# Optimization experiments

Hardware: AMD Instinct MI355X
Metric: run time of the kernel (lower is better)

Reference implementation:

```python
import jax, jax.numpy as jnp
import numpy as np

LN_EPS = 1e-5  # torch LayerNorm default


def layer_norm(x, g, b):
    m = jnp.mean(x, axis=-1, keepdims=True)
    v = jnp.mean((x - m) ** 2, axis=-1, keepdims=True)
    return (x - m) / jnp.sqrt(v + LN_EPS) * g + b


def scatter_mean(src, idx, n):
    # src: [E, h], idx: [E] -> [n, h], mean with count clamped to >= 1
    s = jax.ops.segment_sum(src, idx, num_segments=n)
    cnt = jax.ops.segment_sum(jnp.ones((src.shape[0],), src.dtype), idx, num_segments=n)
    return s / jnp.clip(cnt, 1.0)[:, None]


def setup_inputs() -> dict:
    key = jax.random.key(0)
    ks = jax.random.split(key, 16)
    N, C, E, h = 200000, 50000, 600000, 128

    def w(k, shape, fan_in):
        return (jax.random.normal(k, shape, jnp.float32) / np.float32(np.sqrt(fan_in)))

    ci = jax.random.randint(ks[2], (E,), 0, C)
    vi = jax.random.randint(ks[3], (E,), 0, N)
    return {
        "vh": jax.random.normal(ks[0], (N, h), jnp.float32),
        "ch": jax.random.normal(ks[1], (C, h), jnp.float32),
        "edge_index": jnp.stack([ci, vi]).astype(jnp.int64),
        "ew": jax.random.normal(ks[4], (E,), jnp.float32),
        "v2c_lin_w": w(ks[5], (h, h), h), "v2c_lin_b": jnp.zeros((h,), jnp.float32),
        "v2c_gate_w": w(ks[6], (h, 1), 1), "v2c_gate_b": jnp.zeros((h,), jnp.float32),
        "v2c_upd_w": w(ks[7], (h, 2 * h), 2 * h), "v2c_upd_b": jnp.zeros((h,), jnp.float32),
        "v2c_ln_g": jnp.ones((h,), jnp.float32), "v2c_ln_b": jnp.zeros((h,), jnp.float32),
        "c2v_lin_w": w(ks[8], (h, h), h), "c2v_lin_b": jnp.zeros((h,), jnp.float32),
        "c2v_gate_w": w(ks[9], (h, 1), 1), "c2v_gate_b": jnp.zeros((h,), jnp.float32),
        "c2v_upd_w": w(ks[10], (h, 2 * h), 2 * h), "c2v_upd_b": jnp.zeros((h,), jnp.float32),
        "c2v_ln_g": jnp.ones((h,), jnp.float32), "c2v_ln_b": jnp.zeros((h,), jnp.float32),
    }


def reference(vh, ch, edge_index, ew,
              v2c_lin_w, v2c_lin_b, v2c_gate_w, v2c_gate_b,
              v2c_upd_w, v2c_upd_b, v2c_ln_g, v2c_ln_b,
              c2v_lin_w, c2v_lin_b, c2v_gate_w, c2v_gate_b,
              c2v_upd_w, c2v_upd_b, c2v_ln_g, c2v_ln_b):
    ci, vi = edge_index[0], edge_index[1]
    e = ew[:, None]  # [E, 1]

    # var -> con
    gate = jax.nn.sigmoid(e @ v2c_gate_w.T + v2c_gate_b)          # [E, h]
    msg = (vh @ v2c_lin_w.T + v2c_lin_b)[vi] * gate               # gather + gate
    agg = scatter_mean(msg, ci, ch.shape[0])                      # [C, h]
    ch_new = jax.nn.relu(layer_norm(
        jnp.concatenate([agg, ch], -1) @ v2c_upd_w.T + v2c_upd_b,
        v2c_ln_g, v2c_ln_b))

    # con -> var (uses updated ch)
    gate = jax.nn.sigmoid(e @ c2v_gate_w.T + c2v_gate_b)
    msg = (ch_new @ c2v_lin_w.T + c2v_lin_b)[ci] * gate
    agg = scatter_mean(msg, vi, vh.shape[0])                      # [N, h]
    vh_new = jax.nn.relu(layer_norm(
        jnp.concatenate([agg, vh], -1) @ c2v_upd_w.T + c2v_upd_b,
        c2v_ln_g, c2v_ln_b))

    return vh_new, ch_new
```

## Files before the change

kernel.cpp:

```cpp
#include <hip/hip_runtime.h>

#define LN_EPS 1e-5f

typedef float f32x4 __attribute__((ext_vector_type(4)));
typedef short bf16x8 __attribute__((ext_vector_type(8)));
typedef unsigned short u16x4 __attribute__((ext_vector_type(4)));

__device__ __forceinline__ unsigned short f2bf(float f) {
  unsigned int u = __float_as_uint(f);
  u = (u + 0x7fffu + ((u >> 16) & 1u)) >> 16;
  return (unsigned short)u;
}
__device__ __forceinline__ float bf2f(unsigned short h) {
  return __uint_as_float((unsigned int)h << 16);
}
__device__ __forceinline__ float sigm(float x) {
  return 1.f / (1.f + __expf(-x));
}

__global__ __launch_bounds__(256) void cvt4_bf16(const float* __restrict__ a,
                                                 const float* __restrict__ b,
                                                 const float* __restrict__ c,
                                                 const float* __restrict__ d,
                                                 unsigned short* __restrict__ oa,
                                                 unsigned short* __restrict__ ob,
                                                 unsigned short* __restrict__ oc,
                                                 unsigned short* __restrict__ od) {
  int i = blockIdx.x * 256 + threadIdx.x;
  if (i < 16384) oa[i] = f2bf(a[i]);
  else if (i < 49152) ob[i - 16384] = f2bf(b[i - 16384]);
  else if (i < 65536) oc[i - 49152] = f2bf(c[i - 49152]);
  else if (i < 98304) od[i - 65536] = f2bf(d[i - 65536]);
}

__global__ __launch_bounds__(256) void hist2_rank(const int* __restrict__ ci,
                                                  const int* __restrict__ vi,
                                                  int* __restrict__ cntC,
                                                  int* __restrict__ cntV,
                                                  int* __restrict__ rankC,
                                                  int* __restrict__ rankV, int E) {
  int tid = blockIdx.x * 256 + threadIdx.x;
  int T = gridDim.x * 256;
  int e[4], c[4], v[4];
  bool ok[4];
#pragma unroll
  for (int i = 0; i < 4; ++i) {
    e[i] = tid + i * T;
    ok[i] = e[i] < E;
  }
#pragma unroll
  for (int i = 0; i < 4; ++i) if (ok[i]) c[i] = ci[e[i]];
#pragma unroll
  for (int i = 0; i < 4; ++i) if (ok[i]) v[i] = vi[e[i]];
  int rc[4], rv[4];
#pragma unroll
  for (int i = 0; i < 4; ++i) if (ok[i]) rc[i] = atomicAdd(&cntC[c[i]], 1);
#pragma unroll
  for (int i = 0; i < 4; ++i) if (ok[i]) rv[i] = atomicAdd(&cntV[v[i]], 1);
#pragma unroll
  for (int i = 0; i < 4; ++i) if (ok[i]) rankC[e[i]] = rc[i];
#pragma unroll
  for (int i = 0; i < 4; ++i) if (ok[i]) rankV[e[i]] = rv[i];
}

__global__ __launch_bounds__(256) void scan1(const int* __restrict__ cnt,
                                             int* __restrict__ off,
                                             int* __restrict__ bsum, int M) {
  __shared__ int s[256];
  int base = blockIdx.x * 1024 + threadIdx.x * 4;
  int v[4];
  int tot = 0;
#pragma unroll
  for (int i = 0; i < 4; ++i) {
    int idx = base + i;
    v[i] = (idx < M) ? cnt[idx] : 0;
    tot += v[i];
  }
  s[threadIdx.x] = tot;
  __syncthreads();
  for (int d = 1; d < 256; d <<= 1) {
    int t = (threadIdx.x >= d) ? s[threadIdx.x - d] : 0;
    __syncthreads();
    s[threadIdx.x] += t;
    __syncthreads();
  }
  int excl = s[threadIdx.x] - tot;
#pragma unroll
  for (int i = 0; i < 4; ++i) {
    int idx = base + i;
    if (idx < M) off[idx] = excl;
    excl += v[i];
  }
  if (threadIdx.x == 255) bsum[blockIdx.x] = s[255];
}

__global__ __launch_bounds__(256) void scan2(int* __restrict__ bsum, int nb) {
  __shared__ int s[256];
  __shared__ int carry;
  if (threadIdx.x == 0) carry = 0;
  __syncthreads();
  for (int base = 0; base < nb; base += 256) {
    int idx = base + threadIdx.x;
    int v = (idx < nb) ? bsum[idx] : 0;
    s[threadIdx.x] = v;
    __syncthreads();
    for (int d = 1; d < 256; d <<= 1) {
      int t = (threadIdx.x >= d) ? s[threadIdx.x - d] : 0;
      __syncthreads();
      s[threadIdx.x] += t;
      __syncthreads();
    }
    if (idx < nb) bsum[idx] = s[threadIdx.x] - v + carry;
    __syncthreads();
    if (threadIdx.x == 0) carry += s[255];
    __syncthreads();
  }
}

__global__ __launch_bounds__(256) void scan3(int* __restrict__ off,
                                             const int* __restrict__ bsum, int M, int E) {
  int idx = blockIdx.x * 256 + threadIdx.x;
  if (idx < M) off[idx] += bsum[idx >> 10];
  if (idx == M) off[M] = E;
}

__global__ __launch_bounds__(256) void scatter2_kernel(const int* __restrict__ ci,
                                                       const int* __restrict__ vi,
                                                       const float* __restrict__ ew,
                                                       const int* __restrict__ offC,
                                                       const int* __restrict__ offV,
                                                       const int* __restrict__ rankC,
                                                       const int* __restrict__ rankV,
                                                       int2* __restrict__ edataC,
                                                       int2* __restrict__ edataV, int E) {
  int tid = blockIdx.x * 256 + threadIdx.x;
  int T = gridDim.x * 256;
  int e[4], c[4], v[4], wb[4], rc[4], rv[4];
  bool ok[4];
#pragma unroll
  for (int i = 0; i < 4; ++i) {
    e[i] = tid + i * T;
    ok[i] = e[i] < E;
  }
#pragma unroll
  for (int i = 0; i < 4; ++i) if (ok[i]) c[i] = ci[e[i]];
#pragma unroll
  for (int i = 0; i < 4; ++i) if (ok[i]) v[i] = vi[e[i]];
#pragma unroll
  for (int i = 0; i < 4; ++i) if (ok[i]) wb[i] = __float_as_int(ew[e[i]]);
#pragma unroll
  for (int i = 0; i < 4; ++i) if (ok[i]) rc[i] = rankC[e[i]];
#pragma unroll
  for (int i = 0; i < 4; ++i) if (ok[i]) rv[i] = rankV[e[i]];
  int pc[4], pv[4];
#pragma unroll
  for (int i = 0; i < 4; ++i) if (ok[i]) pc[i] = offC[c[i]] + rc[i];
#pragma unroll
  for (int i = 0; i < 4; ++i) if (ok[i]) pv[i] = offV[v[i]] + rv[i];
#pragma unroll
  for (int i = 0; i < 4; ++i) if (ok[i]) edataC[pc[i]] = make_int2(v[i], wb[i]);
#pragma unroll
  for (int i = 0; i < 4; ++i) if (ok[i]) edataV[pv[i]] = make_int2(c[i], wb[i]);
}

__global__ __launch_bounds__(256) void seg_reduce(const int* __restrict__ off,
                                                  const int2* __restrict__ edata,
                                                  const float* __restrict__ gw,
                                                  const float* __restrict__ gb,
                                                  const unsigned short* __restrict__ src,
                                                  int srcStride,
                                                  unsigned short* __restrict__ out,
                                                  int outStride, int M) {
  int seg = blockIdx.x * 4 + (threadIdx.x >> 6);
  if (seg >= M) return;
  int j = threadIdx.x & 63;
  int start = off[seg], end = off[seg + 1];
  float gwa = gw[2 * j], gwb = gw[2 * j + 1];
  float gba = gb[2 * j], gbb = gb[2 * j + 1];
  float a0 = 0.f, a1 = 0.f;
  int p = start;
  for (; p + 4 <= end; p += 4) {
    int2 e0 = edata[p], e1 = edata[p + 1], e2 = edata[p + 2], e3 = edata[p + 3];
    unsigned int v0 = *reinterpret_cast<const unsigned int*>(&src[(size_t)e0.x * srcStride + 2 * j]);
    unsigned int v1 = *reinterpret_cast<const unsigned int*>(&src[(size_t)e1.x * srcStride + 2 * j]);
    unsigned int v2 = *reinterpret_cast<const unsigned int*>(&src[(size_t)e2.x * srcStride + 2 * j]);
    unsigned int v3 = *reinterpret_cast<const unsigned int*>(&src[(size_t)e3.x * srcStride + 2 * j]);
    float w0 = __int_as_float(e0.y), w1 = __int_as_float(e1.y);
    float w2 = __int_as_float(e2.y), w3 = __int_as_float(e3.y);
    a0 += bf2f((unsigned short)(v0 & 0xffff)) * sigm(w0 * gwa + gba)
        + bf2f((unsigned short)(v1 & 0xffff)) * sigm(w1 * gwa + gba)
        + bf2f((unsigned short)(v2 & 0xffff)) * sigm(w2 * gwa + gba)
        + bf2f((unsigned short)(v3 & 0xffff)) * sigm(w3 * gwa + gba);
    a1 += bf2f((unsigned short)(v0 >> 16)) * sigm(w0 * gwb + gbb)
        + bf2f((unsigned short)(v1 >> 16)) * sigm(w1 * gwb + gbb)
        + bf2f((unsigned short)(v2 >> 16)) * sigm(w2 * gwb + gbb)
        + bf2f((unsigned short)(v3 >> 16)) * sigm(w3 * gwb + gbb);
  }
  if (p + 2 <= end) {
    int2 e0 = edata[p], e1 = edata[p + 1];
    unsigned int v0 = *reinterpret_cast<const unsigned int*>(&src[(size_t)e0.x * srcStride + 2 * j]);
    unsigned int v1 = *reinterpret_cast<const unsigned int*>(&src[(size_t)e1.x * srcStride + 2 * j]);
    float w0 = __int_as_float(e0.y), w1 = __int_as_float(e1.y);
    a0 += bf2f((unsigned short)(v0 & 0xffff)) * sigm(w0 * gwa + gba)
        + bf2f((unsigned short)(v1 & 0xffff)) * sigm(w1 * gwa + gba);
    a1 += bf2f((unsigned short)(v0 >> 16)) * sigm(w0 * gwb + gbb)
        + bf2f((unsigned short)(v1 >> 16)) * sigm(w1 * gwb + gbb);
    p += 2;
  }
  if (p < end) {
    int2 e0 = edata[p];
    unsigned int v0 = *reinterpret_cast<const unsigned int*>(&src[(size_t)e0.x * srcStride + 2 * j]);
    float w0 = __int_as_float(e0.y);
    a0 += bf2f((unsigned short)(v0 & 0xffff)) * sigm(w0 * gwa + gba);
    a1 += bf2f((unsigned short)(v0 >> 16)) * sigm(w0 * gwb + gbb);
  }
  int cnt = end - start;
  float inv = 1.f / (float)(cnt > 1 ? cnt : 1);
  unsigned int packed = (unsigned int)f2bf(a0 * inv) | ((unsigned int)f2bf(a1 * inv) << 16);
  *reinterpret_cast<unsigned int*>(&out[(size_t)seg * outStride + 2 * j]) = packed;
}

template <int K, int OS, bool WBF>
__global__ __launch_bounds__(256) void gemm_lin_mfma(const float* __restrict__ X,
                                                     const unsigned short* __restrict__ Wbf,
                                                     const float* __restrict__ bias,
                                                     unsigned short* __restrict__ out,
                                                     unsigned short* __restrict__ bfdst,
                                                     int M) {
  __shared__ unsigned short Xs[64][40];
  __shared__ unsigned short Bs[128][40];
  const int tid = threadIdx.x;
  const int lane = tid & 63, wv = tid >> 6;
  const int lr = lane & 15, lg = lane >> 4;
  const int row0 = blockIdx.x * 64;

  f32x4 acc[4][2];
#pragma unroll
  for (int mf = 0; mf < 4; ++mf)
#pragma unroll
    for (int nf = 0; nf < 2; ++nf) acc[mf][nf] = (f32x4)(0.f);

  for (int k0 = 0; k0 < K; k0 += 32) {
#pragma unroll
    for (int it = 0; it < 2; ++it) {
      int q = tid + it * 256;
      int r = q >> 3, kq = (q & 7) * 4;
      int grow = row0 + r;
      float4 v = make_float4(0.f, 0.f, 0.f, 0.f);
      if (grow < M) v = *reinterpret_cast<const float4*>(&X[(size_t)grow * K + k0 + kq]);
      u16x4 p = {f2bf(v.x), f2bf(v.y), f2bf(v.z), f2bf(v.w)};
      *reinterpret_cast<u16x4*>(&Xs[r][kq]) = p;
      if (WBF && grow < M)
        *reinterpret_cast<u16x4*>(&bfdst[(size_t)grow * 256 + 128 + k0 + kq]) = p;
    }
#pragma unroll
    for (int it = 0; it < 2; ++it) {
      int q = tid + it * 256;
      int n = q >> 2, kq = (q & 3) * 8;
      bf16x8 wrow = *reinterpret_cast<const bf16x8*>(&Wbf[(size_t)n * K + k0 + kq]);
      *reinterpret_cast<bf16x8*>(&Bs[n][kq]) = wrow;
    }
    __syncthreads();
    bf16x8 a[4], b[2];
#pragma unroll
    for (int mf = 0; mf < 4; ++mf)
      a[mf] = *reinterpret_cast<const bf16x8*>(&Xs[mf * 16 + lr][lg * 8]);
#pragma unroll
    for (int nf = 0; nf < 2; ++nf)
      b[nf] = *reinterpret_cast<const bf16x8*>(&Bs[wv * 32 + nf * 16 + lr][lg * 8]);
#pragma unroll
    for (int mf = 0; mf < 4; ++mf)
#pragma unroll
      for (int nf = 0; nf < 2; ++nf)
        acc[mf][nf] = __builtin_amdgcn_mfma_f32_16x16x32_bf16(a[mf], b[nf], acc[mf][nf], 0, 0, 0);
    __syncthreads();
  }

  int col[2];
  float bv[2];
#pragma unroll
  for (int nf = 0; nf < 2; ++nf) {
    col[nf] = wv * 32 + nf * 16 + lr;
    bv[nf] = bias[col[nf]];
  }
#pragma unroll
  for (int mf = 0; mf < 4; ++mf)
#pragma unroll
    for (int reg = 0; reg < 4; ++reg) {
      int grow = row0 + mf * 16 + lg * 4 + reg;
      if (grow < M) {
#pragma unroll
        for (int nf = 0; nf < 2; ++nf)
          out[(size_t)grow * OS + col[nf]] = f2bf(acc[mf][nf][reg] + bv[nf]);
      }
    }
}

__global__ __launch_bounds__(256) void gemm_upd_mix(const unsigned short* __restrict__ agg,
                                                    const float* __restrict__ base,
                                                    const unsigned short* __restrict__ Wbf,
                                                    const float* __restrict__ bias,
                                                    const float* __restrict__ lng,
                                                    const float* __restrict__ lnb,
                                                    float* __restrict__ out, int M) {
  constexpr int K = 256;
  __shared__ unsigned short Xs[64][40];
  __shared__ unsigned short Bs[128][40];
  __shared__ float sredS[64][4];
  __shared__ float sredQ[64][4];
  const int tid = threadIdx.x;
  const int lane = tid & 63, wv = tid >> 6;
  const int lr = lane & 15, lg = lane >> 4;
  const int row0 = blockIdx.x * 64;

  f32x4 acc[4][2];
#pragma unroll
  for (int mf = 0; mf < 4; ++mf)
#pragma unroll
    for (int nf = 0; nf < 2; ++nf) acc[mf][nf] = (f32x4)(0.f);

  for (int k0 = 0; k0 < K; k0 += 32) {
#pragma unroll
    for (int it = 0; it < 2; ++it) {
      int q = tid + it * 256;
      int r = q >> 3, kq = (q & 7) * 4;
      int grow = row0 + r, gk = k0 + kq;
      u16x4 p = {0, 0, 0, 0};
      if (grow < M) {
        if (gk < 128) {
          p = *reinterpret_cast<const u16x4*>(&agg[(size_t)grow * 128 + gk]);
        } else {
          float4 v = *reinterpret_cast<const float4*>(&base[(size_t)grow * 128 + (gk - 128)]);
          p = {f2bf(v.x), f2bf(v.y), f2bf(v.z), f2bf(v.w)};
        }
      }
      *reinterpret_cast<u16x4*>(&Xs[r][kq]) = p;
    }
#pragma unroll
    for (int it = 0; it < 2; ++it) {
      int q = tid + it * 256;
      int n = q >> 2, kq = (q & 3) * 8;
      bf16x8 wrow = *reinterpret_cast<const bf16x8*>(&Wbf[(size_t)n * K + k0 + kq]);
      *reinterpret_cast<bf16x8*>(&Bs[n][kq]) = wrow;
    }
    __syncthreads();
    bf16x8 a[4], b[2];
#pragma unroll
    for (int mf = 0; mf < 4; ++mf)
      a[mf] = *reinterpret_cast<const bf16x8*>(&Xs[mf * 16 + lr][lg * 8]);
#pragma unroll
    for (int nf = 0; nf < 2; ++nf)
      b[nf] = *reinterpret_cast<const bf16x8*>(&Bs[wv * 32 + nf * 16 + lr][lg * 8]);
#pragma unroll
    for (int mf = 0; mf < 4; ++mf)
#pragma unroll
      for (int nf = 0; nf < 2; ++nf)
        acc[mf][nf] = __builtin_amdgcn_mfma_f32_16x16x32_bf16(a[mf], b[nf], acc[mf][nf], 0, 0, 0);
    __syncthreads();
  }

  int col[2];
  float bv[2], gv[2], lv[2];
#pragma unroll
  for (int nf = 0; nf < 2; ++nf) {
    col[nf] = wv * 32 + nf * 16 + lr;
    bv[nf] = bias[col[nf]];
    gv[nf] = lng[col[nf]];
    lv[nf] = lnb[col[nf]];
  }

  float z[4][4][2];
#pragma unroll
  for (int mf = 0; mf < 4; ++mf)
#pragma unroll
    for (int reg = 0; reg < 4; ++reg) {
      float z0 = acc[mf][0][reg] + bv[0];
      float z1 = acc[mf][1][reg] + bv[1];
      z[mf][reg][0] = z0;
      z[mf][reg][1] = z1;
      float s = z0 + z1;
      float q = z0 * z0 + z1 * z1;
#pragma unroll
      for (int m = 1; m < 16; m <<= 1) {
        s += __shfl_xor(s, m);
        q += __shfl_xor(q, m);
      }
      if (lr == 0) {
        sredS[mf * 16 + lg * 4 + reg][wv] = s;
        sredQ[mf * 16 + lg * 4 + reg][wv] = q;
      }
    }
  __syncthreads();
#pragma unroll
  for (int mf = 0; mf < 4; ++mf)
#pragma unroll
    for (int reg = 0; reg < 4; ++reg) {
      int tr = mf * 16 + lg * 4 + reg;
      f32x4 S4 = *reinterpret_cast<const f32x4*>(&sredS[tr][0]);
      f32x4 Q4 = *reinterpret_cast<const f32x4*>(&sredQ[tr][0]);
      float S = S4[0] + S4[1] + S4[2] + S4[3];
      float Q = Q4[0] + Q4[1] + Q4[2] + Q4[3];
      float mean = S * (1.f / 128.f);
      float var = Q * (1.f / 128.f) - mean * mean;
      float rstd = rsqrtf(var + LN_EPS);
      int grow = row0 + tr;
      if (grow < M) {
#pragma unroll
        for (int nf = 0; nf < 2; ++nf) {
          float y = (z[mf][reg][nf] - mean) * rstd * gv[nf] + lv[nf];
          out[(size_t)grow * 128 + col[nf]] = fmaxf(y, 0.f);
        }
      }
    }
}

__global__ __launch_bounds__(256) void gemm_upd_cat(const unsigned short* __restrict__ Xc,
                                                    const unsigned short* __restrict__ Wbf,
                                                    const float* __restrict__ bias,
                                                    const float* __restrict__ lng,
                                                    const float* __restrict__ lnb,
                                                    float* __restrict__ out, int M) {
  constexpr int K = 256;
  __shared__ unsigned short Xs[64][40];
  __shared__ unsigned short Bs[128][40];
  __shared__ float sredS[64][4];
  __shared__ float sredQ[64][4];
  const int tid = threadIdx.x;
  const int lane = tid & 63, wv = tid >> 6;
  const int lr = lane & 15, lg = lane >> 4;
  const int row0 = blockIdx.x * 64;

  f32x4 acc[4][2];
#pragma unroll
  for (int mf = 0; mf < 4; ++mf)
#pragma unroll
    for (int nf = 0; nf < 2; ++nf) acc[mf][nf] = (f32x4)(0.f);

  for (int k0 = 0; k0 < K; k0 += 32) {
#pragma unroll
    for (int it = 0; it < 2; ++it) {
      int q = tid + it * 256;
      int r = q >> 3, kq = (q & 7) * 4;
      int grow = row0 + r;
      u16x4 p = {0, 0, 0, 0};
      if (grow < M) p = *reinterpret_cast<const u16x4*>(&Xc[(size_t)grow * 256 + k0 + kq]);
      *reinterpret_cast<u16x4*>(&Xs[r][kq]) = p;
    }
#pragma unroll
    for (int it = 0; it < 2; ++it) {
      int q = tid + it * 256;
      int n = q >> 2, kq = (q & 3) * 8;
      bf16x8 wrow = *reinterpret_cast<const bf16x8*>(&Wbf[(size_t)n * K + k0 + kq]);
      *reinterpret_cast<bf16x8*>(&Bs[n][kq]) = wrow;
    }
    __syncthreads();
    bf16x8 a[4], b[2];
#pragma unroll
    for (int mf = 0; mf < 4; ++mf)
      a[mf] = *reinterpret_cast<const bf16x8*>(&Xs[mf * 16 + lr][lg * 8]);
#pragma unroll
    for (int nf = 0; nf < 2; ++nf)
      b[nf] = *reinterpret_cast<const bf16x8*>(&Bs[wv * 32 + nf * 16 + lr][lg * 8]);
#pragma unroll
    for (int mf = 0; mf < 4; ++mf)
#pragma unroll
      for (int nf = 0; nf < 2; ++nf)
        acc[mf][nf] = __builtin_amdgcn_mfma_f32_16x16x32_bf16(a[mf], b[nf], acc[mf][nf], 0, 0, 0);
    __syncthreads();
  }

  int col[2];
  float bv[2], gv[2], lv[2];
#pragma unroll
  for (int nf = 0; nf < 2; ++nf) {
    col[nf] = wv * 32 + nf * 16 + lr;
    bv[nf] = bias[col[nf]];
    gv[nf] = lng[col[nf]];
    lv[nf] = lnb[col[nf]];
  }

  float z[4][4][2];
#pragma unroll
  for (int mf = 0; mf < 4; ++mf)
#pragma unroll
    for (int reg = 0; reg < 4; ++reg) {
      float z0 = acc[mf][0][reg] + bv[0];
      float z1 = acc[mf][1][reg] + bv[1];
      z[mf][reg][0] = z0;
      z[mf][reg][1] = z1;
      float s = z0 + z1;
      float q = z0 * z0 + z1 * z1;
#pragma unroll
      for (int m = 1; m < 16; m <<= 1) {
        s += __shfl_xor(s, m);
        q += __shfl_xor(q, m);
      }
      if (lr == 0) {
        sredS[mf * 16 + lg * 4 + reg][wv] = s;
        sredQ[mf * 16 + lg * 4 + reg][wv] = q;
      }
    }
  __syncthreads();
#pragma unroll
  for (int mf = 0; mf < 4; ++mf)
#pragma unroll
    for (int reg = 0; reg < 4; ++reg) {
      int tr = mf * 16 + lg * 4 + reg;
      f32x4 S4 = *reinterpret_cast<const f32x4*>(&sredS[tr][0]);
      f32x4 Q4 = *reinterpret_cast<const f32x4*>(&sredQ[tr][0]);
      float S = S4[0] + S4[1] + S4[2] + S4[3];
      float Q = Q4[0] + Q4[1] + Q4[2] + Q4[3];
      float mean = S * (1.f / 128.f);
      float var = Q * (1.f / 128.f) - mean * mean;
      float rstd = rsqrtf(var + LN_EPS);
      int grow = row0 + tr;
      if (grow < M) {
#pragma unroll
        for (int nf = 0; nf < 2; ++nf) {
          float y = (z[mf][reg][nf] - mean) * rstd * gv[nf] + lv[nf];
          out[(size_t)grow * 128 + col[nf]] = fmaxf(y, 0.f);
        }
      }
    }
}

extern "C" void kernel_launch(void* const* d_in, const int* in_sizes, int n_in,
                              void* d_out, int out_size, void* d_ws, size_t ws_size,
                              hipStream_t stream) {
  const float* vh = (const float*)d_in[0];
  const float* ch = (const float*)d_in[1];
  const int* ei = (const int*)d_in[2];
  const float* ew = (const float*)d_in[3];
  const float* v2c_lin_w = (const float*)d_in[4];
  const float* v2c_lin_b = (const float*)d_in[5];
  const float* v2c_gate_w = (const float*)d_in[6];
  const float* v2c_gate_b = (const float*)d_in[7];
  const float* v2c_upd_w = (const float*)d_in[8];
  const float* v2c_upd_b = (const float*)d_in[9];
  const float* v2c_ln_g = (const float*)d_in[10];
  const float* v2c_ln_b = (const float*)d_in[11];
  const float* c2v_lin_w = (const float*)d_in[12];
  const float* c2v_lin_b = (const float*)d_in[13];
  const float* c2v_gate_w = (const float*)d_in[14];
  const float* c2v_gate_b = (const float*)d_in[15];
  const float* c2v_upd_w = (const float*)d_in[16];
  const float* c2v_upd_b = (const float*)d_in[17];
  const float* c2v_ln_g = (const float*)d_in[18];
  const float* c2v_ln_b = (const float*)d_in[19];

  const int N = in_sizes[0] / 128;
  const int C = in_sizes[1] / 128;
  const int E = in_sizes[3];
  const int* ci = ei;
  const int* vi = ei + E;

  unsigned short* Xcat = (unsigned short*)d_ws;
  unsigned short* aggC = Xcat + (size_t)N * 256;
  unsigned short* wbf = aggC + (size_t)C * 128;
  unsigned short* wbfLinV = wbf;
  unsigned short* wbfUpdV = wbf + 16384;
  unsigned short* wbfLinC = wbf + 49152;
  unsigned short* wbfUpdC = wbf + 65536;
  int* offC = (int*)(wbf + 98304);
  int* offV = offC + (C + 1);
  size_t ofs = (size_t)((offV + (N + 1)) - (int*)d_ws);
  ofs = (ofs + 1) & ~(size_t)1;
  int2* edataC = (int2*)((int*)d_ws + ofs);
  int2* edataV = edataC + E;
  int* cntC = (int*)aggC;
  int* cntV = cntC + C;
  int* bsumS = cntV + N;
  int* rankC = bsumS + 1024;
  int* rankV = rankC + E;

  float* vhNew = (float*)d_out;
  float* chNew = (float*)d_out + (size_t)N * 128;

  cvt4_bf16<<<(98304 + 255) / 256, 256, 0, stream>>>(v2c_lin_w, v2c_upd_w, c2v_lin_w,
                                                     c2v_upd_w, wbfLinV, wbfUpdV, wbfLinC,
                                                     wbfUpdC);

  const int egrid4 = (E + 4 * 256 - 1) / (4 * 256);

  hipMemsetAsync(cntC, 0, (size_t)(C + N) * sizeof(int), stream);
  hist2_rank<<<egrid4, 256, 0, stream>>>(ci, vi, cntC, cntV, rankC, rankV, E);
  {
    int nb = (C + 1023) / 1024;
    scan1<<<nb, 256, 0, stream>>>(cntC, offC, bsumS, C);
    scan2<<<1, 256, 0, stream>>>(bsumS, nb);
    scan3<<<(C + 1 + 255) / 256, 256, 0, stream>>>(offC, bsumS, C, E);
  }
  {
    int nb = (N + 1023) / 1024;
    scan1<<<nb, 256, 0, stream>>>(cntV, offV, bsumS, N);
    scan2<<<1, 256, 0, stream>>>(bsumS, nb);
    scan3<<<(N + 1 + 255) / 256, 256, 0, stream>>>(offV, bsumS, N, E);
  }
  scatter2_kernel<<<egrid4, 256, 0, stream>>>(ci, vi, ew, offC, offV, rankC, rankV,
                                              edataC, edataV, E);

  gemm_lin_mfma<128, 256, true><<<(N + 63) / 64, 256, 0, stream>>>(vh, wbfLinV, v2c_lin_b,
                                                                   Xcat, Xcat, N);
  seg_reduce<<<(C + 3) / 4, 256, 0, stream>>>(offC, edataC, v2c_gate_w, v2c_gate_b,
                                              Xcat, 256, aggC, 128, C);
  gemm_upd_mix<<<(C + 63) / 64, 256, 0, stream>>>(aggC, ch, wbfUpdV, v2c_upd_b,
                                                  v2c_ln_g, v2c_ln_b, chNew, C);

  unsigned short* tmpC = aggC;
  gemm_lin_mfma<128, 128, false><<<(C + 63) / 64, 256, 0, stream>>>(chNew, wbfLinC,
                                                                    c2v_lin_b, tmpC,
                                                                    nullptr, C);
  seg_reduce<<<(N + 3) / 4, 256, 0, stream>>>(offV, edataV, c2v_gate_w, c2v_gate_b,
                                              tmpC, 128, Xcat, 256, N);
  gemm_upd_cat<<<(N + 63) / 64, 256, 0, stream>>>(Xcat, wbfUpdC, c2v_upd_b,
                                                  c2v_ln_g, c2v_ln_b, vhNew, N);
}
```

Measured before the change: 355.0 us.

## Restructure GEMMs to keep A fragments in registers and stage full weight in LDS

Replaces the K-looped shared-memory GEMMs with kernels where each wave loads its 16 rows of A directly into registers as MFMA fragments and the whole weight matrix (or half of it) is staged once into LDS. Each wave now covers all 128 output columns, so the LayerNorm row reduction is done with in-wave shuffles and no longer needs the cross-wave shared-memory reduction or the per-K-step barriers. The update GEMM uses 512-thread blocks of 128 rows. This trades larger LDS use (about 34KB per block) and more registers for fewer barriers and less A traffic through LDS, which may lower occupancy.

```diff
diff --git a/kernel.cpp b/kernel.cpp
--- a/kernel.cpp
+++ b/kernel.cpp
@@ -220,308 +220,192 @@
   *reinterpret_cast<unsigned int*>(&out[(size_t)seg * outStride + 2 * j]) = packed;
 }
 
-template <int K, int OS, bool WBF>
-__global__ __launch_bounds__(256) void gemm_lin_mfma(const float* __restrict__ X,
-                                                     const unsigned short* __restrict__ Wbf,
-                                                     const float* __restrict__ bias,
-                                                     unsigned short* __restrict__ out,
-                                                     unsigned short* __restrict__ bfdst,
-                                                     int M) {
-  __shared__ unsigned short Xs[64][40];
-  __shared__ unsigned short Bs[128][40];
+template <int OS, bool WBF>
+__global__ __launch_bounds__(256) void gemm_lin_reg(const float* __restrict__ X,
+                                                    const unsigned short* __restrict__ Wbf,
+                                                    const float* __restrict__ bias,
+                                                    unsigned short* __restrict__ out,
+                                                    unsigned short* __restrict__ bfdst,
+                                                    int M) {
+  __shared__ unsigned short Bs[128][136];
   const int tid = threadIdx.x;
   const int lane = tid & 63, wv = tid >> 6;
   const int lr = lane & 15, lg = lane >> 4;
-  const int row0 = blockIdx.x * 64;
-
-  f32x4 acc[4][2];
-#pragma unroll
-  for (int mf = 0; mf < 4; ++mf)
-#pragma unroll
-    for (int nf = 0; nf < 2; ++nf) acc[mf][nf] = (f32x4)(0.f);
-
-  for (int k0 = 0; k0 < K; k0 += 32) {
-#pragma unroll
-    for (int it = 0; it < 2; ++it) {
-      int q = tid + it * 256;
-      int r = q >> 3, kq = (q & 7) * 4;
-      int grow = row0 + r;
-      float4 v = make_float4(0.f, 0.f, 0.f, 0.f);
-      if (grow < M) v = *reinterpret_cast<const float4*>(&X[(size_t)grow * K + k0 + kq]);
-      u16x4 p = {f2bf(v.x), f2bf(v.y), f2bf(v.z), f2bf(v.w)};
-      *reinterpret_cast<u16x4*>(&Xs[r][kq]) = p;
-      if (WBF && grow < M)
-        *reinterpret_cast<u16x4*>(&bfdst[(size_t)grow * 256 + 128 + k0 + kq]) = p;
-    }
-#pragma unroll
-    for (int it = 0; it < 2; ++it) {
-      int q = tid + it * 256;
-      int n = q >> 2, kq = (q & 3) * 8;
-      bf16x8 wrow = *reinterpret_cast<const bf16x8*>(&Wbf[(size_t)n * K + k0 + kq]);
-      *reinterpret_cast<bf16x8*>(&Bs[n][kq]) = wrow;
-    }
-    __syncthreads();
-    bf16x8 a[4], b[2];
-#pragma unroll
-    for (int mf = 0; mf < 4; ++mf)
-      a[mf] = *reinterpret_cast<const bf16x8*>(&Xs[mf * 16 + lr][lg * 8]);
-#pragma unroll
-    for (int nf = 0; nf < 2; ++nf)
-      b[nf] = *reinterpret_cast<const bf16x8*>(&Bs[wv * 32 + nf * 16 + lr][lg * 8]);
-#pragma unroll
-    for (int mf = 0; mf < 4; ++mf)
-#pragma unroll
-      for (int nf = 0; nf < 2; ++nf)
-        acc[mf][nf] = __builtin_amdgcn_mfma_f32_16x16x32_bf16(a[mf], b[nf], acc[mf][nf], 0, 0, 0);
-    __syncthreads();
-  }
-
-  int col[2];
-  float bv[2];
-#pragma unroll
-  for (int nf = 0; nf < 2; ++nf) {
-    col[nf] = wv * 32 + nf * 16 + lr;
-    bv[nf] = bias[col[nf]];
-  }
-#pragma unroll
-  for (int mf = 0; mf < 4; ++mf)
+  const int row0 = blockIdx.x * 64 + wv * 16;
+
+  const int arow = row0 + lr;
+  const bool rowok = arow < M;
+  const float* xrow = X + (size_t)arow * 128;
+
+  float4 x0[4], x1[4];
+#pragma unroll
+  for (int ks = 0; ks < 4; ++ks) {
+    int kb = ks * 32 + lg * 8;
+    if (rowok) {
+      x0[ks] = *reinterpret_cast<const float4*>(xrow + kb);
+      x1[ks] = *reinterpret_cast<const float4*>(xrow + kb + 4);
+    } else {
+      x0[ks] = make_float4(0.f, 0.f, 0.f, 0.f);
+      x1[ks] = x0[ks];
+    }
+  }
+
+#pragma unroll
+  for (int it = 0; it < 8; ++it) {
+    int q = tid + it * 256;
+    int n = q >> 4, kq = (q & 15) * 8;
+    *reinterpret_cast<bf16x8*>(&Bs[n][kq]) =
+        *reinterpret_cast<const bf16x8*>(&Wbf[(size_t)n * 128 + kq]);
+  }
+
+  bf16x8 a[4];
+#pragma unroll
+  for (int ks = 0; ks < 4; ++ks) {
+    a[ks] = (bf16x8){(short)f2bf(x0[ks].x), (short)f2bf(x0[ks].y),
+                     (short)f2bf(x0[ks].z), (short)f2bf(x0[ks].w),
+                     (short)f2bf(x1[ks].x), (short)f2bf(x1[ks].y),
+                     (short)f2bf(x1[ks].z), (short)f2bf(x1[ks].w)};
+    if (WBF && rowok)
+      *reinterpret_cast<bf16x8*>(&bfdst[(size_t)arow * 256 + 128 + ks * 32 + lg * 8]) = a[ks];
+  }
+  __syncthreads();
+
+  f32x4 acc[8];
+#pragma unroll
+  for (int nf = 0; nf < 8; ++nf) acc[nf] = (f32x4)(0.f);
+#pragma unroll
+  for (int ks = 0; ks < 4; ++ks) {
+#pragma unroll
+    for (int nf = 0; nf < 8; ++nf) {
+      bf16x8 b = *reinterpret_cast<const bf16x8*>(&Bs[nf * 16 + lr][ks * 32 + lg * 8]);
+      acc[nf] = __builtin_amdgcn_mfma_f32_16x16x32_bf16(a[ks], b, acc[nf], 0, 0, 0);
+    }
+  }
+
+#pragma unroll
+  for (int nf = 0; nf < 8; ++nf) {
+    int col = nf * 16 + lr;
+    float bv = bias[col];
 #pragma unroll
     for (int reg = 0; reg < 4; ++reg) {
-      int grow = row0 + mf * 16 + lg * 4 + reg;
-      if (grow < M) {
-#pragma unroll
-        for (int nf = 0; nf < 2; ++nf)
-          out[(size_t)grow * OS + col[nf]] = f2bf(acc[mf][nf][reg] + bv[nf]);
-      }
-    }
-}
-
-__global__ __launch_bounds__(256) void gemm_upd_mix(const unsigned short* __restrict__ agg,
+      int grow = row0 + lg * 4 + reg;
+      if (grow < M) out[(size_t)grow * OS + col] = f2bf(acc[nf][reg] + bv);
+    }
+  }
+}
+
+template <bool CAT>
+__global__ __launch_bounds__(512) void gemm_upd_reg(const unsigned short* __restrict__ Xa,
                                                     const float* __restrict__ base,
                                                     const unsigned short* __restrict__ Wbf,
                                                     const float* __restrict__ bias,
                                                     const float* __restrict__ lng,
                                                     const float* __restrict__ lnb,
                                                     float* __restrict__ out, int M) {
-  constexpr int K = 256;
-  __shared__ unsigned short Xs[64][40];
-  __shared__ unsigned short Bs[128][40];
-  __shared__ float sredS[64][4];
-  __shared__ float sredQ[64][4];
+  __shared__ unsigned short Bs[128][136];
   const int tid = threadIdx.x;
   const int lane = tid & 63, wv = tid >> 6;
   const int lr = lane & 15, lg = lane >> 4;
-  const int row0 = blockIdx.x * 64;
-
-  f32x4 acc[4][2];
-#pragma unroll
-  for (int mf = 0; mf < 4; ++mf)
-#pragma unroll
-    for (int nf = 0; nf < 2; ++nf) acc[mf][nf] = (f32x4)(0.f);
-
-  for (int k0 = 0; k0 < K; k0 += 32) {
-#pragma unroll
-    for (int it = 0; it < 2; ++it) {
-      int q = tid + it * 256;
-      int r = q >> 3, kq = (q & 7) * 4;
-      int grow = row0 + r, gk = k0 + kq;
-      u16x4 p = {0, 0, 0, 0};
-      if (grow < M) {
-        if (gk < 128) {
-          p = *reinterpret_cast<const u16x4*>(&agg[(size_t)grow * 128 + gk]);
-        } else {
-          float4 v = *reinterpret_cast<const float4*>(&base[(size_t)grow * 128 + (gk - 128)]);
-          p = {f2bf(v.x), f2bf(v.y), f2bf(v.z), f2bf(v.w)};
-        }
+  const int row0 = blockIdx.x * 128 + wv * 16;
+  const int arow = row0 + lr;
+  const bool rowok = arow < M;
+
+  bf16x8 a[8];
+  if constexpr (CAT) {
+    const unsigned short* xr = Xa + (size_t)arow * 256;
+#pragma unroll
+    for (int ks = 0; ks < 8; ++ks)
+      a[ks] = rowok ? *reinterpret_cast<const bf16x8*>(xr + ks * 32 + lg * 8) : (bf16x8)(short)0;
+  } else {
+    const unsigned short* ar = Xa + (size_t)arow * 128;
+#pragma unroll
+    for (int ks = 0; ks < 4; ++ks)
+      a[ks] = rowok ? *reinterpret_cast<const bf16x8*>(ar + ks * 32 + lg * 8) : (bf16x8)(short)0;
+    const float* br = base + (size_t)arow * 128;
+#pragma unroll
+    for (int ks = 4; ks < 8; ++ks) {
+      float4 f0 = make_float4(0.f, 0.f, 0.f, 0.f), f1 = f0;
+      if (rowok) {
+        int kb = (ks - 4) * 32 + lg * 8;
+        f0 = *reinterpret_cast<const float4*>(br + kb);
+        f1 = *reinterpret_cast<const float4*>(br + kb + 4);
       }
-      *reinterpret_cast<u16x4*>(&Xs[r][kq]) = p;
-    }
-#pragma unroll
-    for (int it = 0; it < 2; ++it) {
-      int q = tid + it * 256;
-      int n = q >> 2, kq = (q & 3) * 8;
-      bf16x8 wrow = *reinterpret_cast<const bf16x8*>(&Wbf[(size_t)n * K + k0 + kq]);
-      *reinterpret_cast<bf16x8*>(&Bs[n][kq]) = wrow;
-    }
-    __syncthreads();
-    bf16x8 a[4], b[2];
-#pragma unroll
-    for (int mf = 0; mf < 4; ++mf)
-      a[mf] = *reinterpret_cast<const bf16x8*>(&Xs[mf * 16 + lr][lg * 8]);
-#pragma unroll
-    for (int nf = 0; nf < 2; ++nf)
-      b[nf] = *reinterpret_cast<const bf16x8*>(&Bs[wv * 32 + nf * 16 + lr][lg * 8]);
-#pragma unroll
-    for (int mf = 0; mf < 4; ++mf)
-#pragma unroll
-      for (int nf = 0; nf < 2; ++nf)
-        acc[mf][nf] = __builtin_amdgcn_mfma_f32_16x16x32_bf16(a[mf], b[nf], acc[mf][nf], 0, 0, 0);
-    __syncthreads();
-  }
-
-  int col[2];
-  float bv[2], gv[2], lv[2];
-#pragma unroll
-  for (int nf = 0; nf < 2; ++nf) {
-    col[nf] = wv * 32 + nf * 16 + lr;
-    bv[nf] = bias[col[nf]];
-    gv[nf] = lng[col[nf]];
-    lv[nf] = lnb[col[nf]];
-  }
-
-  float z[4][4][2];
-#pragma unroll
-  for (int mf = 0; mf < 4; ++mf)
-#pragma unroll
-    for (int reg = 0; reg < 4; ++reg) {
-      float z0 = acc[mf][0][reg] + bv[0];
-      float z1 = acc[mf][1][reg] + bv[1];
-      z[mf][reg][0] = z0;
-      z[mf][reg][1] = z1;
-      float s = z0 + z1;
-      float q = z0 * z0 + z1 * z1;
-#pragma unroll
-      for (int m = 1; m < 16; m <<= 1) {
-        s += __shfl_xor(s, m);
-        q += __shfl_xor(q, m);
+      a[ks] = (bf16x8){(short)f2bf(f0.x), (short)f2bf(f0.y), (short)f2bf(f0.z), (short)f2bf(f0.w),
+                       (short)f2bf(f1.x), (short)f2bf(f1.y), (short)f2bf(f1.z), (short)f2bf(f1.w)};
+    }
+  }
+
+  auto stageW = [&](int kh) {
+#pragma unroll
+    for (int it = 0; it < 4; ++it) {
+      int q = tid + it * 512;
+      int n = q >> 4, kq = (q & 15) * 8;
+      *reinterpret_cast<bf16x8*>(&Bs[n][kq]) =
+          *reinterpret_cast<const bf16x8*>(&Wbf[(size_t)n * 256 + kh * 128 + kq]);
+    }
+  };
+
+  f32x4 acc[8];
+#pragma unroll
+  for (int nf = 0; nf < 8; ++nf) acc[nf] = (f32x4)(0.f);
+
+  stageW(0);
+  __syncthreads();
+#pragma unroll
+  for (int ks = 0; ks < 4; ++ks) {
+#pragma unroll
+    for (int nf = 0; nf < 8; ++nf) {
+      bf16x8 b = *reinterpret_cast<const bf16x8*>(&Bs[nf * 16 + lr][ks * 32 + lg * 8]);
+      acc[nf] = __builtin_amdgcn_mfma_f32_16x16x32_bf16(a[ks], b, acc[nf], 0, 0, 0);
+    }
+  }
+  __syncthreads();
+  stageW(1);
+  __syncthreads();
+#pragma unroll
+  for (int ks = 4; ks < 8; ++ks) {
+#pragma unroll
+    for (int nf = 0; nf < 8; ++nf) {
+      bf16x8 b = *reinterpret_cast<const bf16x8*>(&Bs[nf * 16 + lr][(ks - 4) * 32 + lg * 8]);
+      acc[nf] = __builtin_amdgcn_mfma_f32_16x16x32_bf16(a[ks], b, acc[nf], 0, 0, 0);
+    }
+  }
+
+  float bv[8], gv[8], lv[8];
+#pragma unroll
+  for (int nf = 0; nf < 8; ++nf) {
+    int col = nf * 16 + lr;
+    bv[nf] = bias[col];
+    gv[nf] = lng[col];
+    lv[nf] = lnb[col];
+  }
+#pragma unroll
+  for (int reg = 0; reg < 4; ++reg) {
+    float z[8];
+    float s = 0.f, q = 0.f;
+#pragma unroll
+    for (int nf = 0; nf < 8; ++nf) {
+      z[nf] = acc[nf][reg] + bv[nf];
+      s += z[nf];
+      q += z[nf] * z[nf];
+    }
+#pragma unroll
+    for (int m = 1; m < 16; m <<= 1) {
+      s += __shfl_xor(s, m);
+      q += __shfl_xor(q, m);
+    }
+    float mean = s * (1.f / 128.f);
+    float var = q * (1.f / 128.f) - mean * mean;
+    float rstd = rsqrtf(var + LN_EPS);
+    int grow = row0 + lg * 4 + reg;
+    if (grow < M) {
+#pragma unroll
+      for (int nf = 0; nf < 8; ++nf) {
+        float y = (z[nf] - mean) * rstd * gv[nf] + lv[nf];
+        out[(size_t)grow * 128 + nf * 16 + lr] = fmaxf(y, 0.f);
       }
-      if (lr == 0) {
-        sredS[mf * 16 + lg * 4 + reg][wv] = s;
-        sredQ[mf * 16 + lg * 4 + reg][wv] = q;
-      }
-    }
-  __syncthreads();
-#pragma unroll
-  for (int mf = 0; mf < 4; ++mf)
-#pragma unroll
-    for (int reg = 0; reg < 4; ++reg) {
-      int tr = mf * 16 + lg * 4 + reg;
-      f32x4 S4 = *reinterpret_cast<const f32x4*>(&sredS[tr][0]);
-      f32x4 Q4 = *reinterpret_cast<const f32x4*>(&sredQ[tr][0]);
-      float S = S4[0] + S4[1] + S4[2] + S4[3];
-      float Q = Q4[0] + Q4[1] + Q4[2] + Q4[3];
-      float mean = S * (1.f / 128.f);
-      float var = Q * (1.f / 128.f) - mean * mean;
-      float rstd = rsqrtf(var + LN_EPS);
-      int grow = row0 + tr;
-      if (grow < M) {
-#pragma unroll
-        for (int nf = 0; nf < 2; ++nf) {
-          float y = (z[mf][reg][nf] - mean) * rstd * gv[nf] + lv[nf];
-          out[(size_t)grow * 128 + col[nf]] = fmaxf(y, 0.f);
-        }
-      }
-    }
-}
-
-__global__ __launch_bounds__(256) void gemm_upd_cat(const unsigned short* __restrict__ Xc,
-                                                    const unsigned short* __restrict__ Wbf,
-                                                    const float* __restrict__ bias,
-                                                    const float* __restrict__ lng,
-                                                    const float* __restrict__ lnb,
-                                                    float* __restrict__ out, int M) {
-  constexpr int K = 256;
-  __shared__ unsigned short Xs[64][40];
-  __shared__ unsigned short Bs[128][40];
-  __shared__ float sredS[64][4];
-  __shared__ float sredQ[64][4];
-  const int tid = threadIdx.x;
-  const int lane = tid & 63, wv = tid >> 6;
-  const int lr = lane & 15, lg = lane >> 4;
-  const int row0 = blockIdx.x * 64;
-
-  f32x4 acc[4][2];
-#pragma unroll
-  for (int mf = 0; mf < 4; ++mf)
-#pragma unroll
-    for (int nf = 0; nf < 2; ++nf) acc[mf][nf] = (f32x4)(0.f);
-
-  for (int k0 = 0; k0 < K; k0 += 32) {
-#pragma unroll
-    for (int it = 0; it < 2; ++it) {
-      int q = tid + it * 256;
-      int r = q >> 3, kq = (q & 7) * 4;
-      int grow = row0 + r;
-      u16x4 p = {0, 0, 0, 0};
-      if (grow < M) p = *reinterpret_cast<const u16x4*>(&Xc[(size_t)grow * 256 + k0 + kq]);
-      *reinterpret_cast<u16x4*>(&Xs[r][kq]) = p;
-    }
-#pragma unroll
-    for (int it = 0; it < 2; ++it) {
-      int q = tid + it * 256;
-      int n = q >> 2, kq = (q & 3) * 8;
-      bf16x8 wrow = *reinterpret_cast<const bf16x8*>(&Wbf[(size_t)n * K + k0 + kq]);
-      *reinterpret_cast<bf16x8*>(&Bs[n][kq]) = wrow;
-    }
-    __syncthreads();
-    bf16x8 a[4], b[2];
-#pragma unroll
-    for (int mf = 0; mf < 4; ++mf)
-      a[mf] = *reinterpret_cast<const bf16x8*>(&Xs[mf * 16 + lr][lg * 8]);
-#pragma unroll
-    for (int nf = 0; nf < 2; ++nf)
-      b[nf] = *reinterpret_cast<const bf16x8*>(&Bs[wv * 32 + nf * 16 + lr][lg * 8]);
-#pragma unroll
-    for (int mf = 0; mf < 4; ++mf)
-#pragma unroll
-      for (int nf = 0; nf < 2; ++nf)
-        acc[mf][nf] = __builtin_amdgcn_mfma_f32_16x16x32_bf16(a[mf], b[nf], acc[mf][nf], 0, 0, 0);
-    __syncthreads();
-  }
-
-  int col[2];
-  float bv[2], gv[2], lv[2];
-#pragma unroll
-  for (int nf = 0; nf < 2; ++nf) {
-    col[nf] = wv * 32 + nf * 16 + lr;
-    bv[nf] = bias[col[nf]];
-    gv[nf] = lng[col[nf]];
-    lv[nf] = lnb[col[nf]];
-  }
-
-  float z[4][4][2];
-#pragma unroll
-  for (int mf = 0; mf < 4; ++mf)
-#pragma unroll
-    for (int reg = 0; reg < 4; ++reg) {
-      float z0 = acc[mf][0][reg] + bv[0];
-      float z1 = acc[mf][1][reg] + bv[1];
-      z[mf][reg][0] = z0;
-      z[mf][reg][1] = z1;
-      float s = z0 + z1;
-      float q = z0 * z0 + z1 * z1;
-#pragma unroll
-      for (int m = 1; m < 16; m <<= 1) {
-        s += __shfl_xor(s, m);
-        q += __shfl_xor(q, m);
-      }
-      if (lr == 0) {
-        sredS[mf * 16 + lg * 4 + reg][wv] = s;
-        sredQ[mf * 16 + lg * 4 + reg][wv] = q;
-      }
-    }
-  __syncthreads();
-#pragma unroll
-  for (int mf = 0; mf < 4; ++mf)
-#pragma unroll
-    for (int reg = 0; reg < 4; ++reg) {
-      int tr = mf * 16 + lg * 4 + reg;
-      f32x4 S4 = *reinterpret_cast<const f32x4*>(&sredS[tr][0]);
-      f32x4 Q4 = *reinterpret_cast<const f32x4*>(&sredQ[tr][0]);
-      float S = S4[0] + S4[1] + S4[2] + S4[3];
-      float Q = Q4[0] + Q4[1] + Q4[2] + Q4[3];
-      float mean = S * (1.f / 128.f);
-      float var = Q * (1.f / 128.f) - mean * mean;
-      float rstd = rsqrtf(var + LN_EPS);
-      int grow = row0 + tr;
-      if (grow < M) {
-#pragma unroll
-        for (int nf = 0; nf < 2; ++nf) {
-          float y = (z[mf][reg][nf] - mean) * rstd * gv[nf] + lv[nf];
-          out[(size_t)grow * 128 + col[nf]] = fmaxf(y, 0.f);
-        }
-      }
-    }
+    }
+  }
 }
 
 extern "C" void kernel_launch(void* const* d_in, const int* in_sizes, int n_in,
@@ -599,19 +483,19 @@
   scatter2_kernel<<<egrid4, 256, 0, stream>>>(ci, vi, ew, offC, offV, rankC, rankV,
                                               edataC, edataV, E);
 
-  gemm_lin_mfma<128, 256, true><<<(N + 63) / 64, 256, 0, stream>>>(vh, wbfLinV, v2c_lin_b,
-                                                                   Xcat, Xcat, N);
+  gemm_lin_reg<256, true><<<(N + 63) / 64, 256, 0, stream>>>(vh, wbfLinV, v2c_lin_b,
+                                                             Xcat, Xcat, N);
   seg_reduce<<<(C + 3) / 4, 256, 0, stream>>>(offC, edataC, v2c_gate_w, v2c_gate_b,
                                               Xcat, 256, aggC, 128, C);
-  gemm_upd_mix<<<(C + 63) / 64, 256, 0, stream>>>(aggC, ch, wbfUpdV, v2c_upd_b,
-                                                  v2c_ln_g, v2c_ln_b, chNew, C);
+  gemm_upd_reg<false><<<(C + 127) / 128, 512, 0, stream>>>(aggC, ch, wbfUpdV, v2c_upd_b,
+                                                           v2c_ln_g, v2c_ln_b, chNew, C);
 
   unsigned short* tmpC = aggC;
-  gemm_lin_mfma<128, 128, false><<<(C + 63) / 64, 256, 0, stream>>>(chNew, wbfLinC,
-                                                                    c2v_lin_b, tmpC,
-                                                                    nullptr, C);
+  gemm_lin_reg<128, false><<<(C + 63) / 64, 256, 0, stream>>>(chNew, wbfLinC, c2v_lin_b,
+                                                              tmpC, nullptr, C);
   seg_reduce<<<(N + 3) / 4, 256, 0, stream>>>(offV, edataV, c2v_gate_w, c2v_gate_b,
                                               tmpC, 128, Xcat, 256, N);
-  gemm_upd_cat<<<(N + 63) / 64, 256, 0, stream>>>(Xcat, wbfUpdC, c2v_upd_b,
-                                                  c2v_ln_g, c2v_ln_b, vhNew, N);
-}
+  gemm_upd_reg<true><<<(N + 127) / 128, 512, 0, stream>>>(Xcat, nullptr, wbfUpdC,
+                                                          c2v_upd_b, c2v_ln_g, c2v_ln_b,
+                                                          vhNew, N);
+}
```

New measurement: 336.8 us. 1.05x faster.
